# Kernel optimization log

Hardware: AMD Instinct MI355X
Metric: run time of the kernel (lower is better)

The kernel has to match this reference:

```python
import jax, jax.numpy as jnp
import numpy as np

L, B, P, D, H, DH, KV, M, S, A = 12, 8, 800, 1024, 8, 256, 1, 4096, 50, 32
ROPE_BASE = 10000.0
NEG = -1e30


def _rms(x, w):
    return (x * jax.lax.rsqrt(jnp.mean(x * x, -1, keepdims=True) + 1e-6)) * (1.0 + w)


def _rope(x, cos, sin):
    # x: [B,h,S,DH]; cos/sin: [B,1,S,DH//2]
    x1, x2 = jnp.split(x, 2, axis=-1)
    return jnp.concatenate([x1 * cos - x2 * sin, x2 * cos + x1 * sin], -1)


def setup_inputs() -> dict:
    key = jax.random.key(0)
    ks = iter(jax.random.split(key, 40))
    def nrm(shape, s=0.02):
        return jax.random.normal(next(ks), shape, jnp.float32) * s
    return {
        'prefix_pad_masks': jnp.ones((B, P), jnp.bool_),
        'x_t': jax.random.normal(next(ks), (B, S, A), jnp.float32),
        'timestep': jax.random.uniform(next(ks), (B,), jnp.float32),
        'dt': jnp.full((1,), 0.1, jnp.float32),
        'cache_k': nrm((L, B, KV, P, DH), 1.0),
        'cache_v': nrm((L, B, KV, P, DH), 1.0),
        'w_act_in': nrm((A, D)), 'b_act_in': jnp.zeros((D,), jnp.float32),
        'w_t1': nrm((D, D)), 'b_t1': jnp.zeros((D,), jnp.float32),
        'w_t2': nrm((D, D)), 'b_t2': jnp.zeros((D,), jnp.float32),
        'ln1_w': jnp.zeros((L, D), jnp.float32),
        'ada1_w': nrm((L, D, D)),
        'ln2_w': jnp.zeros((L, D), jnp.float32),
        'wq': nrm((L, D, H * DH)), 'wk': nrm((L, D, KV * DH)),
        'wv': nrm((L, D, KV * DH)), 'wo': nrm((L, H * DH, D)),
        'wg': nrm((L, D, M)), 'wu': nrm((L, D, M)), 'wd': nrm((L, M, D)),
        'lnf_w': jnp.zeros((D,), jnp.float32), 'adaf_w': nrm((D, D)),
        'w_act_out': nrm((D, A)), 'b_act_out': jnp.zeros((A,), jnp.float32),
    }


def reference(prefix_pad_masks, x_t, timestep, dt, cache_k, cache_v,
              w_act_in, b_act_in, w_t1, b_t1, w_t2, b_t2,
              ln1_w, ada1_w, ln2_w, wq, wk, wv, wo, wg, wu, wd,
              lnf_w, adaf_w, w_act_out, b_act_out):
    b, s, _ = x_t.shape
    p = prefix_pad_masks.shape[1]
    # --- embed_suffix: action projection + sinusoidal time -> MLP -> adaRMS cond ---
    suffix = x_t @ w_act_in + b_act_in                              # [B,S,D]
    half = D // 2
    freqs = jnp.exp(-jnp.log(jnp.float32(10000.0)) * jnp.arange(half, dtype=jnp.float32) / half)
    ang = timestep[:, None] * freqs[None, :]
    temb = jnp.concatenate([jnp.sin(ang), jnp.cos(ang)], -1)        # [B,D]
    cond = jax.nn.silu(temb @ w_t1 + b_t1) @ w_t2 + b_t2            # adarms_cond [B,D]
    # --- prefix-suffix 2D attention mask (make_att_2d_masks_trt) ---
    suffix_pad = jnp.ones((b, s), jnp.int32)
    suffix_att = jnp.concatenate([jnp.ones((b, 1), jnp.int32), jnp.zeros((b, s - 1), jnp.int32)], 1)
    cums = jnp.cumsum(suffix_att, 1)
    att2d = cums[:, None, :] <= cums[:, :, None]
    pad2d = (suffix_pad[:, None, :] * suffix_pad[:, :, None]).astype(bool)
    pre2d = jnp.broadcast_to(prefix_pad_masks[:, None, :], (b, s, p))
    full = jnp.concatenate([pre2d, att2d & pad2d], 2)               # [B,S,P+S]
    bias = jnp.where(full, 0.0, NEG)[:, None, :, :].astype(jnp.float32)
    # --- position ids: prefix offset + suffix cumsum - 1 ---
    offs = jnp.sum(prefix_pad_masks.astype(jnp.int32), -1)[:, None]
    pos = offs + jnp.cumsum(suffix_pad, 1) - 1                      # [B,S]
    inv = 1.0 / (ROPE_BASE ** (jnp.arange(0, DH, 2, dtype=jnp.float32) / DH))
    rang = pos[..., None].astype(jnp.float32) * inv                 # [B,S,DH/2]
    cos = jnp.cos(rang)[:, None]
    sin = jnp.sin(rang)[:, None]
    # --- gemma expert (eager attention over KV cache + suffix) ---
    h = suffix * jnp.sqrt(jnp.float32(D))
    def layer(hc, xs):
        l1, a1, l2, Wq, Wk, Wv, Wo, Wg, Wu, Wd, ck, cv = xs
        x = _rms(hc, l1) * (1.0 + (cond @ a1)[:, None, :])
        q = (x @ Wq).reshape(b, s, H, DH).transpose(0, 2, 1, 3)
        k = (x @ Wk).reshape(b, s, KV, DH).transpose(0, 2, 1, 3)
        v = (x @ Wv).reshape(b, s, KV, DH).transpose(0, 2, 1, 3)
        q = _rope(q, cos, sin)
        k = _rope(k, cos, sin)
        kf = jnp.repeat(jnp.concatenate([ck, k], 2), H // KV, 1)    # [B,H,P+S,DH]
        vf = jnp.repeat(jnp.concatenate([cv, v], 2), H // KV, 1)
        sc = jnp.einsum('bhsd,bhtd->bhst', q, kf) / jnp.sqrt(jnp.float32(DH)) + bias
        at = jax.nn.softmax(sc, -1)
        o = jnp.einsum('bhst,bhtd->bhsd', at, vf).transpose(0, 2, 1, 3).reshape(b, s, H * DH)
        hc = hc + o @ Wo
        x2 = _rms(hc, l2)
        hc = hc + (jax.nn.gelu(x2 @ Wg, approximate=True) * (x2 @ Wu)) @ Wd
        return hc, None
    h, _ = jax.lax.scan(layer, h, (ln1_w, ada1_w, ln2_w, wq, wk, wv, wo, wg, wu, wd, cache_k, cache_v))
    hf = _rms(h, lnf_w) * (1.0 + (cond @ adaf_w)[:, None, :])
    v_t = hf[:, -S:].astype(jnp.float32) @ w_act_out + b_act_out    # action_out_proj
    return x_t + dt.reshape(1, 1, 1) * v_t                          # Euler step
```

## Files before the change

kernel.cpp:

```cpp
#include <hip/hip_runtime.h>
#include <hip/hip_bf16.h>
#include <math.h>

#define NLAYER 12
#define NB 8
#define NP 800
#define ND 1024
#define NH 8
#define NDH 256
#define NM 4096
#define NS 50
#define NA 32
#define NKEYS 850
#define KPAD 1024

typedef unsigned short ushort_t;
typedef unsigned int u32;
using f32x4  = __attribute__((ext_vector_type(4))) float;
using short8 = __attribute__((ext_vector_type(8))) short;

__device__ __forceinline__ u32 pack_bf2(float lo, float hi) {
  u32 a = __float_as_uint(lo);
  u32 b = __float_as_uint(hi);
  a += 0x7fffu + ((a >> 16) & 1u);
  b += 0x7fffu + ((b >> 16) & 1u);
  return (a >> 16) | (b & 0xffff0000u);
}
__device__ __forceinline__ ushort_t bf1(float x) {
  u32 a = __float_as_uint(x);
  a += 0x7fffu + ((a >> 16) & 1u);
  return (ushort_t)(a >> 16);
}
__device__ __forceinline__ float ubf(ushort_t h) {
  return __uint_as_float(((u32)h) << 16);
}
__device__ __forceinline__ void async_cp16(const void* g, const void* l) {
  __builtin_amdgcn_global_load_lds(
      (const __attribute__((address_space(1))) u32*)g,
      (__attribute__((address_space(3))) u32*)l, 16, 0, 0);
}
#define SWZ(row, c) ((c) ^ (((row) & 7) << 3))


__global__ void cvt_permute_kernel(const float* __restrict__ src, ushort_t* __restrict__ dst, long nrows) {
  long idx = (long)blockIdx.x * 256 + threadIdx.x;
  long row = idx >> 5;
  int t = (int)(idx & 31);
  if (row >= nrows) return;
  const float* s = src + row * 256 + t * 4;
  float4 lo = *reinterpret_cast<const float4*>(s);
  float4 hi = *reinterpret_cast<const float4*>(s + 128);
  ushort_t* d = dst + row * 256 + t * 8;
  *reinterpret_cast<uint4*>(d) =
      make_uint4(pack_bf2(lo.x, hi.x), pack_bf2(lo.y, hi.y),
                 pack_bf2(lo.z, hi.z), pack_bf2(lo.w, hi.w));
}

template<int MODE>
__global__ __launch_bounds__(256) void transpose_cvt(
    const float* __restrict__ src, long sz, ushort_t* __restrict__ dst, long dz,
    int R, int C, int ldd, int halfOff) {
  __shared__ float Ls[64][65];
  const float* s = src + (long)blockIdx.z * sz;
  ushort_t* d    = dst + (long)blockIdx.z * dz;
  int c0 = blockIdx.x * 64, r0 = blockIdx.y * 64;
  int t = threadIdx.x;
  int rr = t >> 4;
  int cc = (t & 15) * 4;
#pragma unroll
  for (int j = 0; j < 4; ++j) {
    int rl = rr + j * 16;
    int r = r0 + rl;
    float4 v = make_float4(0.f, 0.f, 0.f, 0.f);
    if (r < R) v = *reinterpret_cast<const float4*>(s + (long)r * C + c0 + cc);
    Ls[rl][cc] = v.x; Ls[rl][cc+1] = v.y; Ls[rl][cc+2] = v.z; Ls[rl][cc+3] = v.w;
  }
  __syncthreads();
  int dr = t >> 2;
  int rc = (t & 3) * 16;
  int cg = c0 + dr;
  long orow;
  if (MODE == 0)      orow = cg;
  else if (MODE == 1) orow = ((long)(cg >> 5) << 6) + (cg & 31) + halfOff;
  else                orow = (long)(cg & ~255) + ((cg & 127) << 1) + ((cg >> 7) & 1);
  ushort_t* drow = d + orow * ldd + r0 + rc;
#pragma unroll
  for (int i = 0; i < 16; i += 2) {
    int sr = r0 + rc + i;
    if (sr < R) {
      u32 p = pack_bf2(Ls[rc + i][dr], Ls[rc + i + 1][dr]);
      *reinterpret_cast<u32*>(drow + i) = p;
    }
  }
}


__global__ void temb_kernel(const float* __restrict__ ts, float* __restrict__ temb) {
  int idx = blockIdx.x * 256 + threadIdx.x;
  if (idx >= NB * ND) return;
  int b = idx >> 10, d = idx & 1023;
  int i = d & 511;
  float f = __expf(-logf(10000.f) * (float)i / 512.f);
  float ang = ts[b] * f;
  temb[idx] = (d < 512) ? sinf(ang) : cosf(ang);
}

__global__ void suffix_kernel(const float* __restrict__ x_t, const float* __restrict__ w,
                              const float* __restrict__ bias, float* __restrict__ h) {
  int m = blockIdx.x;
  __shared__ float xs[NA];
  if (threadIdx.x < NA) xs[threadIdx.x] = x_t[m * NA + threadIdx.x];
  __syncthreads();
  for (int n = threadIdx.x; n < ND; n += 256) {
    float acc = bias[n];
#pragma unroll
    for (int k = 0; k < NA; ++k) acc += xs[k] * w[k * ND + n];
    h[m * ND + n] = acc * 32.0f;
  }
}

__global__ void rope_table_kernel(float* __restrict__ cosT, float* __restrict__ sinT) {
  int idx = blockIdx.x * 256 + threadIdx.x;
  if (idx >= NS * 128) return;
  int s = idx >> 7, i = idx & 127;
  float inv = __expf(-(float)(2 * i) / 256.f * logf(10000.f));
  float ang = (float)(NP + s) * inv;
  cosT[idx] = cosf(ang);
  sinT[idx] = sinf(ang);
}

template<bool BFOUT>
__global__ void rms_kernel(const float* __restrict__ hin, const float* __restrict__ w,
                           const float* __restrict__ ada, void* __restrict__ outv) {
  int m = blockIdx.x;
  int b = m / NS;
  int d0 = threadIdx.x * 4;
  float4 v = *reinterpret_cast<const float4*>(hin + (long)m * ND + d0);
  float ss = v.x*v.x + v.y*v.y + v.z*v.z + v.w*v.w;
#pragma unroll
  for (int off = 32; off > 0; off >>= 1) ss += __shfl_down(ss, off);
  __shared__ float red[4];
  int lane = threadIdx.x & 63, wid = threadIdx.x >> 6;
  if (lane == 0) red[wid] = ss;
  __syncthreads();
  float tot = red[0] + red[1] + red[2] + red[3];
  float r = rsqrtf(tot * (1.f / ND) + 1e-6f);
  float4 wv = *reinterpret_cast<const float4*>(w + d0);
  float4 o;
  o.x = v.x * r * (1.f + wv.x);
  o.y = v.y * r * (1.f + wv.y);
  o.z = v.z * r * (1.f + wv.z);
  o.w = v.w * r * (1.f + wv.w);
  if (ada) {
    float4 av = *reinterpret_cast<const float4*>(ada + (long)b * ND + d0);
    o.x *= (1.f + av.x); o.y *= (1.f + av.y); o.z *= (1.f + av.z); o.w *= (1.f + av.w);
  }
  if (BFOUT) {
    *reinterpret_cast<uint2*>((ushort_t*)outv + (long)m * ND + d0) =
        make_uint2(pack_bf2(o.x, o.y), pack_bf2(o.z, o.w));
  } else {
    *reinterpret_cast<float4*>((float*)outv + (long)m * ND + d0) = o;
  }
}

__global__ void final_fused(const float* __restrict__ hin, const float* __restrict__ lnf,
                            const float* __restrict__ adaf, const float* __restrict__ w,
                            const float* __restrict__ bias, const float* __restrict__ x_t,
                            const float* __restrict__ dt, float* __restrict__ out) {
  int m = blockIdx.x;
  int b = m / NS;
  int d0 = threadIdx.x * 4;
  __shared__ float hfs[ND];
  __shared__ float red[256];
  float4 v = *reinterpret_cast<const float4*>(hin + (long)m * ND + d0);
  float ss = v.x*v.x + v.y*v.y + v.z*v.z + v.w*v.w;
#pragma unroll
  for (int off = 32; off > 0; off >>= 1) ss += __shfl_down(ss, off);
  __shared__ float red4[4];
  int lane = threadIdx.x & 63, wid = threadIdx.x >> 6;
  if (lane == 0) red4[wid] = ss;
  __syncthreads();
  float tot = red4[0] + red4[1] + red4[2] + red4[3];
  float r = rsqrtf(tot * (1.f / ND) + 1e-6f);
  float4 wv = *reinterpret_cast<const float4*>(lnf + d0);
  float4 av = *reinterpret_cast<const float4*>(adaf + (long)b * ND + d0);
  hfs[d0]     = v.x * r * (1.f + wv.x) * (1.f + av.x);
  hfs[d0 + 1] = v.y * r * (1.f + wv.y) * (1.f + av.y);
  hfs[d0 + 2] = v.z * r * (1.f + wv.z) * (1.f + av.z);
  hfs[d0 + 3] = v.w * r * (1.f + wv.w) * (1.f + av.w);
  __syncthreads();
  int a = threadIdx.x & 31;
  int kg = threadIdx.x >> 5;
  float acc = 0.f;
  for (int k = kg; k < ND; k += 8) acc += hfs[k] * w[k * NA + a];
  red[threadIdx.x] = acc;
  __syncthreads();
  if (threadIdx.x < NA) {
    float s = 0.f;
#pragma unroll
    for (int g = 0; g < 8; ++g) s += red[g * 32 + a];
    out[m * NA + a] = x_t[m * NA + a] + dt[0] * (s + bias[a]);
  }
}

__global__ __launch_bounds__(256) void gemm64acc(
    const ushort_t* __restrict__ A,
    const ushort_t* __restrict__ B,
    float* __restrict__ C,
    int M, int N, int K, int lda, int ldb, int ldc, int kpb) {
  const int kbeg = blockIdx.z * kpb;
  const int kend = kbeg + kpb;

  const int m0 = blockIdx.x * 64;
  const int n0 = blockIdx.y * 64;
  const int tid = threadIdx.x;
  const int lane = tid & 63;
  const int wbase = tid & 192;
  const int wid = wbase >> 6;
  const int wm = (wid >> 1) * 32;
  const int wn = (wid & 1) * 32;
  const int l15 = lane & 15;
  const int l4  = lane >> 4;

  __shared__ ushort_t As[2][64 * 64];
  __shared__ ushort_t Bs[2][64 * 64];

  f32x4 acc[2][2] = {};

  const int ci0 = wbase + lane;
  const int row0 = ci0 >> 3;
  const int kc0 = (((ci0 & 7) ^ (row0 & 7)) << 3);
  const int ci1 = 256 + ci0;
  const int row1 = ci1 >> 3;
  const int kc1 = (((ci1 & 7) ^ (row1 & 7)) << 3);
  int gra0 = m0 + row0; if (gra0 > M - 1) gra0 = M - 1;
  int gra1 = m0 + row1; if (gra1 > M - 1) gra1 = M - 1;
  const int n_0 = n0 + row0;
  const int n_1 = n0 + row1;

  auto stage = [&](int buf, int k0) {
    async_cp16(A + (long)gra0 * lda + k0 + kc0, (const char*)As[buf] + ci0 * 16);
    async_cp16(B + (long)n_0 * ldb + k0 + kc0, (const char*)Bs[buf] + ci0 * 16);
    async_cp16(A + (long)gra1 * lda + k0 + kc1, (const char*)As[buf] + ci1 * 16);
    async_cp16(B + (long)n_1 * ldb + k0 + kc1, (const char*)Bs[buf] + ci1 * 16);
  };

  const int nt = (kend - kbeg) >> 6;
  stage(0, kbeg);
  __syncthreads();
  int cur = 0;
  for (int t = 0; t < nt; ++t) {
    if (t + 1 < nt) stage(cur ^ 1, kbeg + (t + 1) * 64);
    const ushort_t* Ac = As[cur];
    const ushort_t* Bc = Bs[cur];
#pragma unroll
    for (int ks = 0; ks < 2; ++ks) {
      short8 af[2], bf[2];
#pragma unroll
      for (int mi = 0; mi < 2; ++mi) {
        int row = wm + mi * 16 + l15;
        af[mi] = *reinterpret_cast<const short8*>(&Ac[row * 64 + SWZ(row, ks * 32 + l4 * 8)]);
      }
#pragma unroll
      for (int ni = 0; ni < 2; ++ni) {
        int row = wn + ni * 16 + l15;
        bf[ni] = *reinterpret_cast<const short8*>(&Bc[row * 64 + SWZ(row, ks * 32 + l4 * 8)]);
      }
#pragma unroll
      for (int mi = 0; mi < 2; ++mi)
#pragma unroll
        for (int ni = 0; ni < 2; ++ni)
          acc[mi][ni] = __builtin_amdgcn_mfma_f32_16x16x32_bf16(af[mi], bf[ni], acc[mi][ni], 0, 0, 0);
    }
    __syncthreads();
    cur ^= 1;
  }

#pragma unroll
  for (int mi = 0; mi < 2; ++mi) {
#pragma unroll
    for (int ni = 0; ni < 2; ++ni) {
      int col = n0 + wn + ni * 16 + l15;
      int rb  = m0 + wm + mi * 16 + l4 * 4;
      if (col >= N) continue;
#pragma unroll
      for (int r = 0; r < 4; ++r) {
        int row = rb + r;
        if (row >= M) continue;
        atomicAdd(&C[(long)row * ldc + col], acc[mi][ni][r]);
      }
    }
  }
}

__global__ __launch_bounds__(256) void gemm64rope(
    const ushort_t* __restrict__ A,
    const ushort_t* __restrict__ B,
    const float* __restrict__ cosT, const float* __restrict__ sinT,
    ushort_t* __restrict__ qTo, ushort_t* __restrict__ k_new,
    ushort_t* __restrict__ vT_l) {
  const int M = 400, lda = 1024, ldb = 1024;
  const int m0 = blockIdx.x * 64;
  const int n0 = blockIdx.y * 64;
  const int tid = threadIdx.x;
  const int lane = tid & 63;
  const int wbase = tid & 192;
  const int wid = wbase >> 6;
  const int wm = (wid >> 1) * 32;
  const int wn = (wid & 1) * 32;
  const int l15 = lane & 15;
  const int l4  = lane >> 4;

  __shared__ ushort_t As[2][64 * 64];
  __shared__ ushort_t Bs[2][64 * 64];

  f32x4 acc[2][2] = {};

  const int ci0 = wbase + lane;
  const int row0 = ci0 >> 3;
  const int kc0 = (((ci0 & 7) ^ (row0 & 7)) << 3);
  const int ci1 = 256 + ci0;
  const int row1 = ci1 >> 3;
  const int kc1 = (((ci1 & 7) ^ (row1 & 7)) << 3);
  int gra0 = m0 + row0; if (gra0 > M - 1) gra0 = M - 1;
  int gra1 = m0 + row1; if (gra1 > M - 1) gra1 = M - 1;
  const int n_0 = n0 + row0;
  const int n_1 = n0 + row1;

  auto stage = [&](int buf, int k0) {
    async_cp16(A + (long)gra0 * lda + k0 + kc0, (const char*)As[buf] + ci0 * 16);
    async_cp16(B + (long)n_0 * ldb + k0 + kc0, (const char*)Bs[buf] + ci0 * 16);
    async_cp16(A + (long)gra1 * lda + k0 + kc1, (const char*)As[buf] + ci1 * 16);
    async_cp16(B + (long)n_1 * ldb + k0 + kc1, (const char*)Bs[buf] + ci1 * 16);
  };

  stage(0, 0);
  __syncthreads();
  int cur = 0;
  for (int t = 0; t < 16; ++t) {
    if (t + 1 < 16) stage(cur ^ 1, (t + 1) * 64);
    const ushort_t* Ac = As[cur];
    const ushort_t* Bc = Bs[cur];
#pragma unroll
    for (int ks = 0; ks < 2; ++ks) {
      short8 af[2], bf[2];
#pragma unroll
      for (int mi = 0; mi < 2; ++mi) {
        int row = wm + mi * 16 + l15;
        af[mi] = *reinterpret_cast<const short8*>(&Ac[row * 64 + SWZ(row, ks * 32 + l4 * 8)]);
      }
#pragma unroll
      for (int ni = 0; ni < 2; ++ni) {
        int row = wn + ni * 16 + l15;
        bf[ni] = *reinterpret_cast<const short8*>(&Bc[row * 64 + SWZ(row, ks * 32 + l4 * 8)]);
      }
#pragma unroll
      for (int mi = 0; mi < 2; ++mi)
#pragma unroll
        for (int ni = 0; ni < 2; ++ni)
          acc[mi][ni] = __builtin_amdgcn_mfma_f32_16x16x32_bf16(af[mi], bf[ni], acc[mi][ni], 0, 0, 0);
    }
    __syncthreads();
    cur ^= 1;
  }

#pragma unroll
  for (int mi = 0; mi < 2; ++mi) {
#pragma unroll
    for (int ni = 0; ni < 2; ++ni) {
      int col = n0 + wn + ni * 16 + l15;
      int rb  = m0 + wm + mi * 16 + l4 * 4;
      float pv[4];
#pragma unroll
      for (int r = 0; r < 4; ++r) pv[r] = __shfl_xor(acc[mi][ni][r], 1);
#pragma unroll
      for (int r = 0; r < 4; ++r) {
        int row = rb + r;
        if (row >= 400) continue;
        int b = row / NS, s = row - b * NS;
        float v = acc[mi][ni][r];
        if (col < 2304) {
          int j = col & 255;
          int i = j >> 1;
          float c = cosT[s * 128 + i], sn = sinT[s * 128 + i];
          float o = (col & 1) ? (v * c + pv[r] * sn) : (v * c - pv[r] * sn);
          if (col < 2048)
            qTo[((long)((b << 3) + (col >> 8)) * NS + s) * 256 + j] = bf1(o);
          else
            k_new[(long)row * 256 + j] = bf1(o);
        } else {
          vT_l[((long)(b * 256 + (col - 2304))) * KPAD + NP + s] = bf1(v);
        }
      }
    }
  }
}

__global__ __launch_bounds__(256) void flash2_kernel(
    const ushort_t* __restrict__ qT,
    const ushort_t* __restrict__ kcache_l,
    const ushort_t* __restrict__ k_new,
    const ushort_t* __restrict__ vT_l,
    const ushort_t* __restrict__ zpad,
    float* __restrict__ opart, float* __restrict__ mpart, float* __restrict__ lpart) {
  const int bh = blockIdx.x;
  const int ch = blockIdx.y;
  const int b  = bh >> 3;
  const int tid = threadIdx.x;
  const int lane = tid & 63;
  const int w = tid >> 6;
  const int wm = (w >> 1) * 32;
  const int wn = (w & 1) * 128;
  const int l15 = lane & 15;
  const int l4  = lane >> 4;

  __shared__ __align__(16) char lds[100352];
  ushort_t* KV0 = (ushort_t*)lds;
  ushort_t* KV1 = (ushort_t*)(lds + 32768);
  ushort_t* Ps  = (ushort_t*)(lds + 65536);
  float* SMm = (float*)(lds + 99328);
  float* SMl = (float*)(lds + 99840);

  short8 qf[4][2][2];
  {
    const ushort_t* qbase = qT + (long)bh * NS * 256;
#pragma unroll
    for (int mi = 0; mi < 2; ++mi) {
      int row = wm + mi * 16 + l15;
      int qr = row < NS ? row : NS - 1;
      const ushort_t* qrow = qbase + (long)qr * 256;
#pragma unroll
      for (int s = 0; s < 4; ++s)
#pragma unroll
        for (int ks = 0; ks < 2; ++ks)
          qf[s][mi][ks] = *reinterpret_cast<const short8*>(qrow + s * 64 + ks * 32 + l4 * 8);
    }
  }

  auto stageK = [&](ushort_t* buf, int s) {
#pragma unroll
    for (int i = 0; i < 8; ++i) {
      int ci = i * 256 + tid;
      int key = ch * 256 + (ci >> 3);
      int seg = (ci ^ (ci >> 3)) & 7;
      const ushort_t* src;
      if (key < NP)         src = kcache_l + ((long)(b * NP + key)) * 256 + s * 64 + seg * 8;
      else if (key < NKEYS) src = k_new + ((long)(b * NS + key - NP)) * 256 + s * 64 + seg * 8;
      else                  src = zpad + seg * 8;
      async_cp16(src, (char*)buf + ci * 16);
    }
  };
  auto stageV = [&](ushort_t* buf, int s) {
#pragma unroll
    for (int i = 0; i < 8; ++i) {
      int ci = i * 256 + tid;
      int dout = ci >> 3;
      int seg = (ci ^ (ci >> 3)) & 7;
      async_cp16(vT_l + ((long)(b * 256 + dout)) * KPAD + ch * 256 + s * 64 + seg * 8,
                 (char*)buf + ci * 16);
    }
  };

  f32x4 s2[2][8] = {};
  stageK(KV0, 0);
  __syncthreads();
#pragma unroll
  for (int s = 0; s < 4; ++s) {
    ushort_t* buf = (s & 1) ? KV1 : KV0;
    ushort_t* nxt = (s & 1) ? KV0 : KV1;
    if (s < 3) stageK(nxt, s + 1);
    __builtin_amdgcn_s_setprio(1);
#pragma unroll
    for (int ks = 0; ks < 2; ++ks) {
      short8 bf[8];
#pragma unroll
      for (int ni = 0; ni < 8; ++ni) {
        int row = wn + ni * 16 + l15;
        bf[ni] = *reinterpret_cast<const short8*>(&buf[row * 64 + SWZ(row, ks * 32 + l4 * 8)]);
      }
#pragma unroll
      for (int mi = 0; mi < 2; ++mi)
#pragma unroll
        for (int ni = 0; ni < 8; ++ni)
          s2[mi][ni] = __builtin_amdgcn_mfma_f32_16x16x32_bf16(qf[s][mi][ks], bf[ni], s2[mi][ni], 0, 0, 0);
    }
    __builtin_amdgcn_s_setprio(0);
    __syncthreads();
  }

  stageV(KV0, 0);

  float mx[2][4];
#pragma unroll
  for (int mi = 0; mi < 2; ++mi)
#pragma unroll
    for (int r = 0; r < 4; ++r) mx[mi][r] = -1e30f;
#pragma unroll
  for (int mi = 0; mi < 2; ++mi)
#pragma unroll
    for (int ni = 0; ni < 8; ++ni) {
      int key = ch * 256 + wn + ni * 16 + l15;
      bool valid = key < NKEYS;
#pragma unroll
      for (int r = 0; r < 4; ++r) {
        float v = s2[mi][ni][r] * 0.0625f;
        v = valid ? v : -1e30f;
        s2[mi][ni][r] = v;
        mx[mi][r] = fmaxf(mx[mi][r], v);
      }
    }
#pragma unroll
  for (int off = 1; off < 16; off <<= 1)
#pragma unroll
    for (int mi = 0; mi < 2; ++mi)
#pragma unroll
      for (int r = 0; r < 4; ++r)
        mx[mi][r] = fmaxf(mx[mi][r], __shfl_xor(mx[mi][r], off));
  if (l15 == 0) {
#pragma unroll
    for (int mi = 0; mi < 2; ++mi)
#pragma unroll
      for (int r = 0; r < 4; ++r)
        SMm[(w & 1) * 64 + wm + mi * 16 + l4 * 4 + r] = mx[mi][r];
  }
  __syncthreads();
  float mrow[2][4], sum[2][4];
#pragma unroll
  for (int mi = 0; mi < 2; ++mi)
#pragma unroll
    for (int r = 0; r < 4; ++r) {
      int row = wm + mi * 16 + l4 * 4 + r;
      mrow[mi][r] = fmaxf(SMm[row], SMm[64 + row]);
      sum[mi][r] = 0.f;
    }
#pragma unroll
  for (int mi = 0; mi < 2; ++mi)
#pragma unroll
    for (int ni = 0; ni < 8; ++ni) {
      int colp = wn + ni * 16 + l15;
#pragma unroll
      for (int r = 0; r < 4; ++r) {
        float e = __expf(s2[mi][ni][r] - mrow[mi][r]);
        Ps[(wm + mi * 16 + l4 * 4 + r) * 264 + colp] = bf1(e);
        sum[mi][r] += e;
      }
    }
#pragma unroll
  for (int off = 1; off < 16; off <<= 1)
#pragma unroll
    for (int mi = 0; mi < 2; ++mi)
#pragma unroll
      for (int r = 0; r < 4; ++r)
        sum[mi][r] += __shfl_xor(sum[mi][r], off);
  if (l15 == 0) {
#pragma unroll
    for (int mi = 0; mi < 2; ++mi)
#pragma unroll
      for (int r = 0; r < 4; ++r)
        SMl[(w & 1) * 64 + wm + mi * 16 + l4 * 4 + r] = sum[mi][r];
  }
  __syncthreads();
  if ((w & 1) == 0 && l15 == 0) {
#pragma unroll
    for (int mi = 0; mi < 2; ++mi)
#pragma unroll
      for (int r = 0; r < 4; ++r) {
        int row = wm + mi * 16 + l4 * 4 + r;
        if (row < NS) {
          mpart[((long)bh * 4 + ch) * NS + row] = mrow[mi][r];
          lpart[((long)bh * 4 + ch) * NS + row] = SMl[row] + SMl[64 + row];
        }
      }
  }

  f32x4 o2[2][8] = {};
#pragma unroll
  for (int s = 0; s < 4; ++s) {
    ushort_t* buf = (s & 1) ? KV1 : KV0;
    ushort_t* nxt = (s & 1) ? KV0 : KV1;
    if (s < 3) stageV(nxt, s + 1);
    __builtin_amdgcn_s_setprio(1);
#pragma unroll
    for (int ks = 0; ks < 2; ++ks) {
      short8 af[2], bf[8];
#pragma unroll
      for (int mi = 0; mi < 2; ++mi)
        af[mi] = *reinterpret_cast<const short8*>(&Ps[(wm + mi * 16 + l15) * 264 + s * 64 + ks * 32 + l4 * 8]);
#pragma unroll
      for (int ni = 0; ni < 8; ++ni) {
        int row = wn + ni * 16 + l15;
        bf[ni] = *reinterpret_cast<const short8*>(&buf[row * 64 + SWZ(row, ks * 32 + l4 * 8)]);
      }
#pragma unroll
      for (int mi = 0; mi < 2; ++mi)
#pragma unroll
        for (int ni = 0; ni < 8; ++ni)
          o2[mi][ni] = __builtin_amdgcn_mfma_f32_16x16x32_bf16(af[mi], bf[ni], o2[mi][ni], 0, 0, 0);
    }
    __builtin_amdgcn_s_setprio(0);
    __syncthreads();
  }

#pragma unroll
  for (int mi = 0; mi < 2; ++mi)
#pragma unroll
    for (int ni = 0; ni < 8; ++ni) {
      int col = wn + ni * 16 + l15;
#pragma unroll
      for (int r = 0; r < 4; ++r) {
        int row = wm + mi * 16 + l4 * 4 + r;
        if (row < NS)
          opart[(((long)bh * 4 + ch) * NS + row) * 256 + col] = o2[mi][ni][r];
      }
    }
}

__global__ void att_combine(const float* __restrict__ opart, const float* __restrict__ mpart,
                            const float* __restrict__ lpart, ushort_t* __restrict__ o_buf) {
  int blk = blockIdx.x;
  int b = blk / NS, s = blk - b * NS;
  int d = threadIdx.x;
  for (int h = 0; h < NH; ++h) {
    int bh = b * NH + h;
    float mv[4];
    float m = -1e30f;
#pragma unroll
    for (int c = 0; c < 4; ++c) {
      mv[c] = mpart[((long)bh * 4 + c) * NS + s];
      m = fmaxf(m, mv[c]);
    }
    float den = 0.f, o = 0.f;
#pragma unroll
    for (int c = 0; c < 4; ++c) {
      float wgt = __expf(mv[c] - m);
      den += wgt * lpart[((long)bh * 4 + c) * NS + s];
      o   += wgt * opart[(((long)bh * 4 + c) * NS + s) * 256 + d];
    }
    o_buf[(long)blk * 2048 + h * 256 + d] = bf1(o / den);
  }
}

__global__ __launch_bounds__(256) void gemm64G(
    const ushort_t* __restrict__ A, const ushort_t* __restrict__ B,
    ushort_t* __restrict__ C, int M, int K, int lda, int ldb, int ldc) {
  const int m0 = blockIdx.x * 64;
  const int n0 = blockIdx.y * 64;
  const int tid = threadIdx.x;
  const int lane = tid & 63;
  const int wbase = tid & 192;
  const int wid = wbase >> 6;
  const int l15 = lane & 15;
  const int l4  = lane >> 4;

  __shared__ ushort_t As[2][64 * 64];
  __shared__ ushort_t Bs[2][64 * 64];

  f32x4 acc[4] = {};

  const int ci0 = wbase + lane;
  const int row0 = ci0 >> 3;
  const int kc0 = (((ci0 & 7) ^ (row0 & 7)) << 3);
  const int ci1 = 256 + ci0;
  const int row1 = ci1 >> 3;
  const int kc1 = (((ci1 & 7) ^ (row1 & 7)) << 3);
  int gra0 = m0 + row0; if (gra0 > M - 1) gra0 = M - 1;
  int gra1 = m0 + row1; if (gra1 > M - 1) gra1 = M - 1;

  auto stage = [&](int buf, int k0) {
    async_cp16(A + (long)gra0 * lda + k0 + kc0, (const char*)As[buf] + ci0 * 16);
    async_cp16(B + (long)(n0 + row0) * ldb + k0 + kc0, (const char*)Bs[buf] + ci0 * 16);
    async_cp16(A + (long)gra1 * lda + k0 + kc1, (const char*)As[buf] + ci1 * 16);
    async_cp16(B + (long)(n0 + row1) * ldb + k0 + kc1, (const char*)Bs[buf] + ci1 * 16);
  };

  const int nt = K >> 6;
  stage(0, 0);
  __syncthreads();
  int cur = 0;
  for (int t = 0; t < nt; ++t) {
    if (t + 1 < nt) stage(cur ^ 1, (t + 1) * 64);
    const ushort_t* Ac = As[cur];
    const ushort_t* Bc = Bs[cur];
#pragma unroll
    for (int ks = 0; ks < 2; ++ks) {
      int arow = wid * 16 + l15;
      short8 af = *reinterpret_cast<const short8*>(&Ac[arow * 64 + SWZ(arow, ks * 32 + l4 * 8)]);
#pragma unroll
      for (int ni = 0; ni < 4; ++ni) {
        int row = ni * 16 + l15;
        short8 bf = *reinterpret_cast<const short8*>(&Bc[row * 64 + SWZ(row, ks * 32 + l4 * 8)]);
        acc[ni] = __builtin_amdgcn_mfma_f32_16x16x32_bf16(af, bf, acc[ni], 0, 0, 0);
      }
    }
    __syncthreads();
    cur ^= 1;
  }

#pragma unroll
  for (int ni = 0; ni < 2; ++ni) {
    int col = (n0 >> 1) + ni * 16 + l15;
    int rb  = m0 + wid * 16 + l4 * 4;
#pragma unroll
    for (int r = 0; r < 4; ++r) {
      int row = rb + r;
      if (row >= M) continue;
      float g = acc[ni][r];
      float u = acc[ni + 2][r];
      float inner = 0.7978845608028654f * (g + 0.044715f * g * g * g);
      float t = 0.5f * g * (1.f + tanhf(inner));
      C[(long)row * ldc + col] = bf1(t * u);
    }
  }
}

template<int EPI>
__global__ __launch_bounds__(256)
void gemm_f32_kernel(const float* __restrict__ A,
                     const float* __restrict__ B1,
                     float* __restrict__ C,
                     int M, int N, int K, int lda, int ldb, int ldc,
                     const float* __restrict__ bias) {
  const int m0 = blockIdx.x * 64;
  const int n0 = blockIdx.y * 64;
  const int tid = threadIdx.x;
  const int lane = tid & 63;
  const int wid = tid >> 6;
  const int wm = (wid >> 1) * 32;
  const int wn = (wid & 1) * 32;
  const int l15 = lane & 15;
  const int l4  = lane >> 4;

  __shared__ __align__(16) ushort_t As[64][72];
  __shared__ __align__(16) ushort_t Bs[64][72];

  f32x4 acc[2][2] = {};

  for (int k0 = 0; k0 < K; k0 += 64) {
#pragma unroll
    for (int pass = 0; pass < 2; ++pass) {
      int c = tid + pass * 256;
      int row = c >> 3;
      int kc = (c & 7) * 8;
      int gr = m0 + row, gk = k0 + kc;
      float v[8];
#pragma unroll
      for (int j = 0; j < 8; ++j)
        v[j] = (gr < M && gk + j < K) ? A[(long)gr * lda + gk + j] : 0.f;
      *reinterpret_cast<uint4*>(&As[row][kc]) =
          make_uint4(pack_bf2(v[0],v[1]), pack_bf2(v[2],v[3]),
                     pack_bf2(v[4],v[5]), pack_bf2(v[6],v[7]));
    }
    {
      int n = tid & 63;
      int kg = tid >> 6;
      int gn = n0 + n;
      u32 pk[8];
#pragma unroll
      for (int kk = 0; kk < 16; kk += 2) {
        int kga = k0 + kg * 16 + kk;
        float v0 = (gn < N && kga < K)     ? B1[(long)kga * ldb + gn] : 0.f;
        float v1 = (gn < N && kga + 1 < K) ? B1[(long)(kga + 1) * ldb + gn] : 0.f;
        pk[kk >> 1] = pack_bf2(v0, v1);
      }
      *reinterpret_cast<uint4*>(&Bs[n][kg * 16])     = make_uint4(pk[0],pk[1],pk[2],pk[3]);
      *reinterpret_cast<uint4*>(&Bs[n][kg * 16 + 8]) = make_uint4(pk[4],pk[5],pk[6],pk[7]);
    }
    __syncthreads();
#pragma unroll
    for (int ks = 0; ks < 2; ++ks) {
      short8 af[2], bfr[2];
#pragma unroll
      for (int mi = 0; mi < 2; ++mi)
        af[mi] = *reinterpret_cast<const short8*>(&As[wm + mi*16 + l15][ks*32 + l4*8]);
#pragma unroll
      for (int ni = 0; ni < 2; ++ni)
        bfr[ni] = *reinterpret_cast<const short8*>(&Bs[wn + ni*16 + l15][ks*32 + l4*8]);
#pragma unroll
      for (int mi = 0; mi < 2; ++mi)
#pragma unroll
        for (int ni = 0; ni < 2; ++ni)
          acc[mi][ni] = __builtin_amdgcn_mfma_f32_16x16x32_bf16(af[mi], bfr[ni], acc[mi][ni], 0, 0, 0);
    }
    __syncthreads();
  }

#pragma unroll
  for (int mi = 0; mi < 2; ++mi) {
#pragma unroll
    for (int ni = 0; ni < 2; ++ni) {
      int col = n0 + wn + ni * 16 + l15;
      int rb  = m0 + wm + mi * 16 + l4 * 4;
#pragma unroll
      for (int r = 0; r < 4; ++r) {
        int row = rb + r;
        if (row < M && col < N) {
          float v = acc[mi][ni][r];
          if (EPI == 1) C[(long)row * ldc + col] = v + bias[col];
          else {
            float t = v + bias[col];
            C[(long)row * ldc + col] = t / (1.f + __expf(-t));
          }
        }
      }
    }
  }
}

__global__ __launch_bounds__(256)
void gemm_f32sk(const float* __restrict__ A,
                const float* __restrict__ B, long bz,
                float* __restrict__ C, long cz,
                int M, int N, int K, int lda, int ldb, int ldc, int nks) {
  const int zz = blockIdx.z;
  const int layer = zz / nks;
  const int chunk = zz % nks;
  const int kpb = K / nks;
  const int kbeg = chunk * kpb, kend = kbeg + kpb;
  const float* Bb = B + (long)layer * bz;
  float* Cb = C + (long)layer * cz;

  const int m0 = blockIdx.x * 64;
  const int n0 = blockIdx.y * 64;
  const int tid = threadIdx.x;
  const int lane = tid & 63;
  const int wid = tid >> 6;
  const int wm = (wid >> 1) * 32;
  const int wn = (wid & 1) * 32;
  const int l15 = lane & 15;
  const int l4  = lane >> 4;

  __shared__ __align__(16) ushort_t As[64][72];
  __shared__ __align__(16) ushort_t Bs[64][72];

  f32x4 acc[2][2] = {};

  for (int k0 = kbeg; k0 < kend; k0 += 64) {
#pragma unroll
    for (int pass = 0; pass < 2; ++pass) {
      int c = tid + pass * 256;
      int row = c >> 3;
      int kc = (c & 7) * 8;
      int gr = m0 + row, gk = k0 + kc;
      float v[8];
#pragma unroll
      for (int j = 0; j < 8; ++j)
        v[j] = (gr < M) ? A[(long)gr * lda + gk + j] : 0.f;
      *reinterpret_cast<uint4*>(&As[row][kc]) =
          make_uint4(pack_bf2(v[0],v[1]), pack_bf2(v[2],v[3]),
                     pack_bf2(v[4],v[5]), pack_bf2(v[6],v[7]));
    }
    {
      int n = tid & 63;
      int kg = tid >> 6;
      int gn = n0 + n;
      u32 pk[8];
#pragma unroll
      for (int kk = 0; kk < 16; kk += 2) {
        int kga = k0 + kg * 16 + kk;
        float v0 = Bb[(long)kga * ldb + gn];
        float v1 = Bb[(long)(kga + 1) * ldb + gn];
        pk[kk >> 1] = pack_bf2(v0, v1);
      }
      *reinterpret_cast<uint4*>(&Bs[n][kg * 16])     = make_uint4(pk[0],pk[1],pk[2],pk[3]);
      *reinterpret_cast<uint4*>(&Bs[n][kg * 16 + 8]) = make_uint4(pk[4],pk[5],pk[6],pk[7]);
    }
    __syncthreads();
#pragma unroll
    for (int ks = 0; ks < 2; ++ks) {
      short8 af[2], bfr[2];
#pragma unroll
      for (int mi = 0; mi < 2; ++mi)
        af[mi] = *reinterpret_cast<const short8*>(&As[wm + mi*16 + l15][ks*32 + l4*8]);
#pragma unroll
      for (int ni = 0; ni < 2; ++ni)
        bfr[ni] = *reinterpret_cast<const short8*>(&Bs[wn + ni*16 + l15][ks*32 + l4*8]);
#pragma unroll
      for (int mi = 0; mi < 2; ++mi)
#pragma unroll
        for (int ni = 0; ni < 2; ++ni)
          acc[mi][ni] = __builtin_amdgcn_mfma_f32_16x16x32_bf16(af[mi], bfr[ni], acc[mi][ni], 0, 0, 0);
    }
    __syncthreads();
  }

#pragma unroll
  for (int mi = 0; mi < 2; ++mi) {
#pragma unroll
    for (int ni = 0; ni < 2; ++ni) {
      int col = n0 + wn + ni * 16 + l15;
      int rb  = m0 + wm + mi * 16 + l4 * 4;
#pragma unroll
      for (int r = 0; r < 4; ++r) {
        int row = rb + r;
        if (row < M && col < N)
          atomicAdd(&Cb[(long)row * ldc + col], acc[mi][ni][r]);
      }
    }
  }
}

extern "C" void kernel_launch(void* const* d_in, const int* in_sizes, int n_in,
                              void* d_out, int out_size, void* d_ws, size_t ws_size,
                              hipStream_t stream) {
  (void)in_sizes; (void)n_in; (void)out_size; (void)ws_size;
  const float* x_t      = (const float*)d_in[1];
  const float* tstep    = (const float*)d_in[2];
  const float* dtp      = (const float*)d_in[3];
  const float* cache_k  = (const float*)d_in[4];
  const float* cache_v  = (const float*)d_in[5];
  const float* w_act_in = (const float*)d_in[6];
  const float* b_act_in = (const float*)d_in[7];
  const float* w_t1     = (const float*)d_in[8];
  const float* b_t1     = (const float*)d_in[9];
  const float* w_t2     = (const float*)d_in[10];
  const float* b_t2     = (const float*)d_in[11];
  const float* ln1_w    = (const float*)d_in[12];
  const float* ada1_w   = (const float*)d_in[13];
  const float* ln2_w    = (const float*)d_in[14];
  const float* wq       = (const float*)d_in[15];
  const float* wk       = (const float*)d_in[16];
  const float* wv       = (const float*)d_in[17];
  const float* wo       = (const float*)d_in[18];
  const float* wg       = (const float*)d_in[19];
  const float* wu       = (const float*)d_in[20];
  const float* wd       = (const float*)d_in[21];
  const float* lnf_w    = (const float*)d_in[22];
  const float* adaf_w   = (const float*)d_in[23];
  const float* wao      = (const float*)d_in[24];
  const float* bao      = (const float*)d_in[25];
  float* outp = (float*)d_out;

  char* p = (char*)d_ws;
  auto alloc = [&](size_t bytes) { char* r = p; p += (bytes + 255) & ~(size_t)255; return r; };

  ushort_t* wqkvT  = (ushort_t*)alloc((size_t)12 * 2560 * 1024 * 2);
  ushort_t* woT    = (ushort_t*)alloc((size_t)12 * 1024 * 2048 * 2);
  ushort_t* wguT   = (ushort_t*)alloc((size_t)12 * 8192 * 1024 * 2);
  ushort_t* wdT    = (ushort_t*)alloc((size_t)12 * 1024 * 4096 * 2);
  ushort_t* kcache = (ushort_t*)alloc((size_t)12 * 8 * NP * 256 * 2);
  ushort_t* vT     = (ushort_t*)alloc((size_t)12 * 8 * 256 * KPAD * 2);
  ushort_t* qT     = (ushort_t*)alloc((size_t)64 * NS * 256 * 2);
  ushort_t* k_new  = (ushort_t*)alloc((size_t)400 * 256 * 2);
  float*    opart  = (float*)alloc((size_t)64 * 4 * NS * 256 * 4);
  float*    mpart  = (float*)alloc((size_t)64 * 4 * NS * 4);
  float*    lpart  = (float*)alloc((size_t)64 * 4 * NS * 4);
  ushort_t* o_buf  = (ushort_t*)alloc((size_t)400 * 2048 * 2);
  ushort_t* t_buf  = (ushort_t*)alloc((size_t)400 * 4096 * 2);
  ushort_t* x_buf  = (ushort_t*)alloc((size_t)400 * 1024 * 2);
  float*    h_buf  = (float*)alloc((size_t)400 * 1024 * 4);
  float*    temb   = (float*)alloc(8 * 1024 * 4);
  float*    tmp    = (float*)alloc(8 * 1024 * 4);
  float*    cond   = (float*)alloc(8 * 1024 * 4);
  float*    ada_all= (float*)alloc((size_t)12 * 8 * 1024 * 4);
  float*    adaf_o = (float*)alloc(8 * 1024 * 4);
  float*    cosT   = (float*)alloc(NS * 128 * 4);
  float*    sinT   = (float*)alloc(NS * 128 * 4);
  ushort_t* zpad   = (ushort_t*)alloc(512 * 2);

  hipMemsetAsync(zpad, 0, 512 * 2, stream);
  hipMemsetAsync(ada_all, 0, ((size_t)12 * 8 * 1024 + 8 * 1024) * 4, stream);

  cvt_permute_kernel<<<9600, 256, 0, stream>>>(cache_k, kcache, (long)12 * 8 * NP);
  transpose_cvt<2><<<dim3(32, 16, 12), 256, 0, stream>>>(wq, (long)1024 * 2048, wqkvT, (long)2560 * 1024, 1024, 2048, 1024, 0);
  transpose_cvt<2><<<dim3(4, 16, 12), 256, 0, stream>>>(wk, (long)1024 * 256, wqkvT + (long)2048 * 1024, (long)2560 * 1024, 1024, 256, 1024, 0);
  transpose_cvt<0><<<dim3(4, 16, 12), 256, 0, stream>>>(wv, (long)1024 * 256, wqkvT + (long)2304 * 1024, (long)2560 * 1024, 1024, 256, 1024, 0);
  transpose_cvt<0><<<dim3(16, 32, 12), 256, 0, stream>>>(wo, (long)2048 * 1024, woT, (long)1024 * 2048, 2048, 1024, 2048, 0);
  transpose_cvt<1><<<dim3(64, 16, 12), 256, 0, stream>>>(wg, (long)1024 * 4096, wguT, (long)8192 * 1024, 1024, 4096, 1024, 0);
  transpose_cvt<1><<<dim3(64, 16, 12), 256, 0, stream>>>(wu, (long)1024 * 4096, wguT, (long)8192 * 1024, 1024, 4096, 1024, 32);
  transpose_cvt<0><<<dim3(16, 64, 12), 256, 0, stream>>>(wd, (long)4096 * 1024, wdT, (long)1024 * 4096, 4096, 1024, 4096, 0);
  transpose_cvt<0><<<dim3(4, 13, 96), 256, 0, stream>>>(cache_v, (long)NP * 256, vT, (long)256 * KPAD, NP, 256, KPAD, 0);

  temb_kernel<<<32, 256, 0, stream>>>(tstep, temb);
  suffix_kernel<<<400, 256, 0, stream>>>(x_t, w_act_in, b_act_in, h_buf);
  rope_table_kernel<<<25, 256, 0, stream>>>(cosT, sinT);
  gemm_f32_kernel<2><<<dim3(1, 16, 1), 256, 0, stream>>>(temb, w_t1, tmp, NB, ND, ND, ND, ND, ND, b_t1);
  gemm_f32_kernel<1><<<dim3(1, 16, 1), 256, 0, stream>>>(tmp, w_t2, cond, NB, ND, ND, ND, ND, ND, b_t2);
  gemm_f32sk<<<dim3(1, 16, 48), 256, 0, stream>>>(cond, ada1_w, (long)ND * ND, ada_all, (long)NB * ND, NB, ND, ND, ND, ND, ND, 4);
  gemm_f32sk<<<dim3(1, 16, 4), 256, 0, stream>>>(cond, adaf_w, 0, adaf_o, 0, NB, ND, ND, ND, ND, ND, 4);

  for (int l = 0; l < NLAYER; ++l) {
    ushort_t* vT_l = vT + (long)l * 8 * 256 * KPAD;
    rms_kernel<true><<<400, 256, 0, stream>>>(h_buf, ln1_w + (long)l * ND, ada_all + (long)l * NB * ND, x_buf);
    gemm64rope<<<dim3(7, 40, 1), 256, 0, stream>>>(
        x_buf, wqkvT + (long)l * 2560 * 1024, cosT, sinT, qT, k_new, vT_l);
    flash2_kernel<<<dim3(64, 4, 1), 256, 0, stream>>>(
        qT, kcache + (long)l * 8 * NP * 256, k_new, vT_l, zpad, opart, mpart, lpart);
    att_combine<<<400, 256, 0, stream>>>(opart, mpart, lpart, o_buf);
    gemm64acc<<<dim3(7, 16, 4), 256, 0, stream>>>(
        o_buf, woT + (long)l * 1024 * 2048, h_buf, 400, 1024, 2048, 2048, 2048, 1024, 512);
    rms_kernel<true><<<400, 256, 0, stream>>>(h_buf, ln2_w + (long)l * ND, nullptr, x_buf);
    gemm64G<<<dim3(7, 128, 1), 256, 0, stream>>>(
        x_buf, wguT + (long)l * 8192 * 1024, t_buf, 400, 1024, 1024, 1024, 4096);
    gemm64acc<<<dim3(7, 16, 4), 256, 0, stream>>>(
        t_buf, wdT + (long)l * 1024 * 4096, h_buf, 400, 1024, 4096, 4096, 4096, 1024, 1024);
  }

  final_fused<<<400, 256, 0, stream>>>(h_buf, lnf_w, adaf_o, wao, bao, x_t, dtp, outp);
}
```

Measured before the change: 1.922 ms.

## Replace split-K atomics with partial slabs reduced in RMS, remap workgroups for XCDs

The split-K output GEMMs now write plain stores into four per-chunk slabs instead of issuing fp32 atomicAdds into the residual. The following RMS kernel (or the final fused kernel) sums the slabs into the residual. GEMM and attention kernels also remap the workgroup ID so that neighbouring tiles land on the same XCD, which is meant to improve L2 reuse. GELU's tanh is rewritten as an exp-based sigmoid form. The cost is extra slab traffic and a larger memory footprint.

Measured after the change: 1.811 ms. 1.06x faster.

```diff
diff --git a/kernel.cpp b/kernel.cpp
--- a/kernel.cpp
+++ b/kernel.cpp
@@ -130,12 +130,21 @@
 }
 
 template<bool BFOUT>
-__global__ void rms_kernel(const float* __restrict__ hin, const float* __restrict__ w,
+__global__ void rms_kernel(float* __restrict__ hin, const float* __restrict__ slabs,
+                           const float* __restrict__ w,
                            const float* __restrict__ ada, void* __restrict__ outv) {
   int m = blockIdx.x;
   int b = m / NS;
   int d0 = threadIdx.x * 4;
   float4 v = *reinterpret_cast<const float4*>(hin + (long)m * ND + d0);
+  if (slabs) {
+#pragma unroll
+    for (int c = 0; c < 4; ++c) {
+      float4 sv = *reinterpret_cast<const float4*>(slabs + ((long)c * 400 + m) * ND + d0);
+      v.x += sv.x; v.y += sv.y; v.z += sv.z; v.w += sv.w;
+    }
+    *reinterpret_cast<float4*>(hin + (long)m * ND + d0) = v;
+  }
   float ss = v.x*v.x + v.y*v.y + v.z*v.z + v.w*v.w;
 #pragma unroll
   for (int off = 32; off > 0; off >>= 1) ss += __shfl_down(ss, off);
@@ -163,7 +172,8 @@
   }
 }
 
-__global__ void final_fused(const float* __restrict__ hin, const float* __restrict__ lnf,
+__global__ void final_fused(const float* __restrict__ hin, const float* __restrict__ slabs,
+                            const float* __restrict__ lnf,
                             const float* __restrict__ adaf, const float* __restrict__ w,
                             const float* __restrict__ bias, const float* __restrict__ x_t,
                             const float* __restrict__ dt, float* __restrict__ out) {
@@ -173,6 +183,11 @@
   __shared__ float hfs[ND];
   __shared__ float red[256];
   float4 v = *reinterpret_cast<const float4*>(hin + (long)m * ND + d0);
+#pragma unroll
+  for (int c = 0; c < 4; ++c) {
+    float4 sv = *reinterpret_cast<const float4*>(slabs + ((long)c * 400 + m) * ND + d0);
+    v.x += sv.x; v.y += sv.y; v.z += sv.z; v.w += sv.w;
+  }
   float ss = v.x*v.x + v.y*v.y + v.z*v.z + v.w*v.w;
 #pragma unroll
   for (int off = 32; off > 0; off >>= 1) ss += __shfl_down(ss, off);
@@ -203,16 +218,20 @@
   }
 }
 
-__global__ __launch_bounds__(256) void gemm64acc(
+__global__ __launch_bounds__(256) void gemm64slab(
     const ushort_t* __restrict__ A,
     const ushort_t* __restrict__ B,
     float* __restrict__ C,
     int M, int N, int K, int lda, int ldb, int ldc, int kpb) {
-  const int kbeg = blockIdx.z * kpb;
+  const int flat3 = blockIdx.x + 7 * (blockIdx.y + 16 * blockIdx.z);
+  const int wgid = (flat3 & 7) * 56 + (flat3 >> 3);
+  const int chunk = wgid / 112;
+  const int rem = wgid - chunk * 112;
+  const int m0 = (rem % 7) * 64;
+  const int n0 = (rem / 7) * 64;
+  const int kbeg = chunk * kpb;
   const int kend = kbeg + kpb;
 
-  const int m0 = blockIdx.x * 64;
-  const int n0 = blockIdx.y * 64;
   const int tid = threadIdx.x;
   const int lane = tid & 63;
   const int wbase = tid & 192;
@@ -276,6 +295,7 @@
     cur ^= 1;
   }
 
+  float* Cs = C + (long)chunk * 400 * ldc;
 #pragma unroll
   for (int mi = 0; mi < 2; ++mi) {
 #pragma unroll
@@ -287,7 +307,7 @@
       for (int r = 0; r < 4; ++r) {
         int row = rb + r;
         if (row >= M) continue;
-        atomicAdd(&C[(long)row * ldc + col], acc[mi][ni][r]);
+        Cs[(long)row * ldc + col] = acc[mi][ni][r];
       }
     }
   }
@@ -300,8 +320,10 @@
     ushort_t* __restrict__ qTo, ushort_t* __restrict__ k_new,
     ushort_t* __restrict__ vT_l) {
   const int M = 400, lda = 1024, ldb = 1024;
-  const int m0 = blockIdx.x * 64;
-  const int n0 = blockIdx.y * 64;
+  const int flat = blockIdx.x + 7 * blockIdx.y;
+  const int wgid = (flat & 7) * 35 + (flat >> 3);
+  const int m0 = (wgid % 7) * 64;
+  const int n0 = (wgid / 7) * 64;
   const int tid = threadIdx.x;
   const int lane = tid & 63;
   const int wbase = tid & 192;
@@ -403,8 +425,10 @@
     const ushort_t* __restrict__ vT_l,
     const ushort_t* __restrict__ zpad,
     float* __restrict__ opart, float* __restrict__ mpart, float* __restrict__ lpart) {
-  const int bh = blockIdx.x;
-  const int ch = blockIdx.y;
+  const int flat = blockIdx.x + 64 * blockIdx.y;
+  const int wgid = (flat & 7) * 32 + (flat >> 3);
+  const int bh = wgid & 63;
+  const int ch = wgid >> 6;
   const int b  = bh >> 3;
   const int tid = threadIdx.x;
   const int lane = tid & 63;
@@ -643,8 +667,10 @@
 __global__ __launch_bounds__(256) void gemm64G(
     const ushort_t* __restrict__ A, const ushort_t* __restrict__ B,
     ushort_t* __restrict__ C, int M, int K, int lda, int ldb, int ldc) {
-  const int m0 = blockIdx.x * 64;
-  const int n0 = blockIdx.y * 64;
+  const int flat = blockIdx.x + 7 * blockIdx.y;
+  const int wgid = (flat & 7) * 112 + (flat >> 3);
+  const int m0 = (wgid % 7) * 64;
+  const int n0 = (wgid / 7) * 64;
   const int tid = threadIdx.x;
   const int lane = tid & 63;
   const int wbase = tid & 192;
@@ -707,7 +733,7 @@
       float g = acc[ni][r];
       float u = acc[ni + 2][r];
       float inner = 0.7978845608028654f * (g + 0.044715f * g * g * g);
-      float t = 0.5f * g * (1.f + tanhf(inner));
+      float t = g / (1.f + __expf(-2.f * inner));
       C[(long)row * ldc + col] = bf1(t * u);
     }
   }
@@ -944,6 +970,8 @@
   float*    opart  = (float*)alloc((size_t)64 * 4 * NS * 256 * 4);
   float*    mpart  = (float*)alloc((size_t)64 * 4 * NS * 4);
   float*    lpart  = (float*)alloc((size_t)64 * 4 * NS * 4);
+  float*    woP    = (float*)alloc((size_t)4 * 400 * 1024 * 4);
+  float*    wdP    = (float*)alloc((size_t)4 * 400 * 1024 * 4);
   ushort_t* o_buf  = (ushort_t*)alloc((size_t)400 * 2048 * 2);
   ushort_t* t_buf  = (ushort_t*)alloc((size_t)400 * 4096 * 2);
   ushort_t* x_buf  = (ushort_t*)alloc((size_t)400 * 1024 * 2);
@@ -980,20 +1008,22 @@
 
   for (int l = 0; l < NLAYER; ++l) {
     ushort_t* vT_l = vT + (long)l * 8 * 256 * KPAD;
-    rms_kernel<true><<<400, 256, 0, stream>>>(h_buf, ln1_w + (long)l * ND, ada_all + (long)l * NB * ND, x_buf);
+    rms_kernel<true><<<400, 256, 0, stream>>>(
+        h_buf, l == 0 ? nullptr : wdP, ln1_w + (long)l * ND, ada_all + (long)l * NB * ND, x_buf);
     gemm64rope<<<dim3(7, 40, 1), 256, 0, stream>>>(
         x_buf, wqkvT + (long)l * 2560 * 1024, cosT, sinT, qT, k_new, vT_l);
     flash2_kernel<<<dim3(64, 4, 1), 256, 0, stream>>>(
         qT, kcache + (long)l * 8 * NP * 256, k_new, vT_l, zpad, opart, mpart, lpart);
     att_combine<<<400, 256, 0, stream>>>(opart, mpart, lpart, o_buf);
-    gemm64acc<<<dim3(7, 16, 4), 256, 0, stream>>>(
-        o_buf, woT + (long)l * 1024 * 2048, h_buf, 400, 1024, 2048, 2048, 2048, 1024, 512);
-    rms_kernel<true><<<400, 256, 0, stream>>>(h_buf, ln2_w + (long)l * ND, nullptr, x_buf);
+    gemm64slab<<<dim3(7, 16, 4), 256, 0, stream>>>(
+        o_buf, woT + (long)l * 1024 * 2048, woP, 400, 1024, 2048, 2048, 2048, 1024, 512);
+    rms_kernel<true><<<400, 256, 0, stream>>>(
+        h_buf, woP, ln2_w + (long)l * ND, nullptr, x_buf);
     gemm64G<<<dim3(7, 128, 1), 256, 0, stream>>>(
         x_buf, wguT + (long)l * 8192 * 1024, t_buf, 400, 1024, 1024, 1024, 4096);
-    gemm64acc<<<dim3(7, 16, 4), 256, 0, stream>>>(
-        t_buf, wdT + (long)l * 1024 * 4096, h_buf, 400, 1024, 4096, 4096, 4096, 1024, 1024);
-  }
-
-  final_fused<<<400, 256, 0, stream>>>(h_buf, lnf_w, adaf_o, wao, bao, x_t, dtp, outp);
-}
+    gemm64slab<<<dim3(7, 16, 4), 256, 0, stream>>>(
+        t_buf, wdT + (long)l * 1024 * 4096, wdP, 400, 1024, 4096, 4096, 4096, 1024, 1024);
+  }
+
+  final_fused<<<400, 256, 0, stream>>>(h_buf, wdP, lnf_w, adaf_o, wao, bao, x_t, dtp, outp);
+}
```
